# Performance work log

Measured on AMD Instinct MI355X. Metric: run time of the kernel, lower is better.

Reference implementation:

```python
import jax, jax.numpy as jnp
import numpy as np

H = 4
N = 1024
E = 4096
LE = 16384
FN = 128
FE = 64
FNO = 128
FEO = 64


def _lin(x, W, b):
    # torch nn.Linear: y = x @ W.T + b, W is [out, in]
    return x @ W.T + b


def setup_inputs() -> dict:
    key = jax.random.key(0)
    ks = jax.random.split(key, 24)
    s = 0.05
    inp = {}
    inp["node_inputs"] = jax.random.normal(ks[0], (N, FN), jnp.float32)
    inp["edge_inputs"] = jax.random.normal(ks[1], (E, FE), jnp.float32)
    inp["src"] = jax.random.randint(ks[2], (E,), 0, N, jnp.int32)
    inp["dst"] = jax.random.randint(ks[3], (E,), 0, N, jnp.int32)
    inp["lg_src"] = jax.random.randint(ks[4], (LE,), 0, E, jnp.int32)
    inp["lg_dst"] = jax.random.randint(ks[5], (LE,), 0, E, jnp.int32)
    # projection linear weights (torch Linear layout [out, in])
    inp["nqW"] = jax.random.normal(ks[6], (H * FN, FN), jnp.float32) * s
    inp["nqb"] = jax.random.normal(ks[7], (H * FN,), jnp.float32) * s
    inp["nkW"] = jax.random.normal(ks[8], (H, FN), jnp.float32) * s
    inp["nkb"] = jax.random.normal(ks[9], (H,), jnp.float32) * s
    inp["nvW"] = jax.random.normal(ks[10], (H * FN, FN), jnp.float32) * s
    inp["nvb"] = jax.random.normal(ks[11], (H * FN,), jnp.float32) * s
    inp["eqW"] = jax.random.normal(ks[12], (H * FE, FE), jnp.float32) * s
    inp["eqb"] = jax.random.normal(ks[13], (H * FE,), jnp.float32) * s
    inp["ekW"] = jax.random.normal(ks[14], (H, FE), jnp.float32) * s
    inp["ekb"] = jax.random.normal(ks[15], (H,), jnp.float32) * s
    inp["evW"] = jax.random.normal(ks[16], (H * FE, FE), jnp.float32) * s
    inp["evb"] = jax.random.normal(ks[17], (H * FE,), jnp.float32) * s
    # convolution output linears
    inp["ncW"] = jax.random.normal(ks[18], (FNO, FN), jnp.float32) * s
    inp["ncb"] = jax.random.normal(ks[19], (FNO,), jnp.float32) * s
    inp["ecW"] = jax.random.normal(ks[20], (FEO, FE), jnp.float32) * s
    inp["ecb"] = jax.random.normal(ks[21], (FEO,), jnp.float32) * s
    return inp


def reference(node_inputs, edge_inputs, src, dst, lg_src, lg_dst,
              nqW, nqb, nkW, nkb, nvW, nvb,
              eqW, eqb, ekW, ekb, evW, evb,
              ncW, ncb, ecW, ecb):
    n, fn = node_inputs.shape
    e, fe = edge_inputs.shape
    # per-head Q/K/V projections; .view(H, -1, F) == row-major reshape
    nq = _lin(node_inputs, nqW, nqb).reshape(H, -1, fn)   # [H,N,FN]
    nk = _lin(node_inputs, nkW, nkb).reshape(H, -1, 1)    # [H,N,1]
    nv = _lin(node_inputs, nvW, nvb).reshape(H, -1, fn)   # [H,N,FN]
    eq = _lin(edge_inputs, eqW, eqb).reshape(H, -1, fe)   # [H,E,FE]
    ek = _lin(edge_inputs, ekW, ekb).reshape(H, -1, 1)    # [H,E,1]
    ev = _lin(edge_inputs, evW, evb).reshape(H, -1, fe)   # [H,E,FE]
    # self attention: softmax(Q @ Q^T @ K, dim=1); associate as Q @ (Q^T K)
    node_sa = jax.nn.softmax(nq @ (jnp.swapaxes(nq, -1, -2) @ nk), axis=1)  # [H,N,1]
    edge_sa = jax.nn.softmax(eq @ (jnp.swapaxes(eq, -1, -2) @ ek), axis=1)  # [H,E,1]
    # vectorized edge-indexed scatter of attention scores into dense projections
    node_proj = jnp.zeros((H, n, n), node_inputs.dtype).at[:, src, dst].set(edge_sa[:, :, 0])
    conn = dst[lg_src]  # g.find_edges(source)[1]: destination node of edge lg_src
    edge_proj = jnp.zeros((H, e, e), edge_inputs.dtype).at[:, lg_src, lg_dst].set(node_sa[:, conn, 0])
    # dense adjacency matrices
    A = jnp.zeros((n, n), node_inputs.dtype).at[src, dst].set(1.0)
    Alg = jnp.zeros((e, e), edge_inputs.dtype).at[lg_src, lg_dst].set(1.0)
    # 'sum' aggregation: (attn_proj * A) @ value, then Linear + relu
    node_out = jax.nn.relu(_lin((node_proj * A) @ nv, ncW, ncb))   # [H,N,FNO]
    edge_out = jax.nn.relu(_lin((edge_proj * Alg) @ ev, ecW, ecb)) # [H,E,FEO]
    return (node_out, edge_out)
```

## Files before the change

kernel.cpp:

```cpp
#include <hip/hip_runtime.h>

#define H_ 4
#define N_ 1024
#define E_ 4096
#define LE_ 16384
#define FN_ 128
#define FE_ 64
#define CAP_ 32

struct P {
  const float *Xn, *Xe;
  const int *src, *dst, *lgs, *lgd;
  const float *nqW, *nqb, *nkW, *nkb, *nvW, *nvb;
  const float *eqW, *eqb, *ekW, *ekb, *evW, *evb;
  const float *ncW, *ncb, *ecW, *ecb;
  float *out;
  float *NV, *EV, *nsa, *esa;
  int *cntN, *cntE;
  int *listN, *listE;
  int *listNc, *listEc;
  int *degN, *degE;
};

template<int K, bool RELU>
__device__ void gemm_tile(const float* __restrict__ X, const float* __restrict__ W,
                          const float* __restrict__ b, float* __restrict__ C,
                          int O, int r0, int o0, float* smem, int t) {
  float* Xs = smem;
  float* Ws = smem + 2048;
  const int tn = t & 15, tm = t >> 4;
  float acc[4][4] = {};
  for (int k0 = 0; k0 < K; k0 += 32) {
#pragma unroll
    for (int ph = 0; ph < 2; ++ph) {
      int i4 = t + ph * 256;
      int m = i4 >> 3;
      int k4 = (i4 & 7) << 2;
      int m4 = m >> 2, ml = m & 3;
      float4 vx = *(const float4*)&X[(r0 + m) * K + k0 + k4];
      float4 vw = *(const float4*)&W[(o0 + m) * K + k0 + k4];
      Xs[(k4 + 0) * 64 + ((m4 ^ ((k4 + 0) & 15)) << 2) + ml] = vx.x;
      Xs[(k4 + 1) * 64 + ((m4 ^ ((k4 + 1) & 15)) << 2) + ml] = vx.y;
      Xs[(k4 + 2) * 64 + ((m4 ^ ((k4 + 2) & 15)) << 2) + ml] = vx.z;
      Xs[(k4 + 3) * 64 + ((m4 ^ ((k4 + 3) & 15)) << 2) + ml] = vx.w;
      Ws[(k4 + 0) * 64 + ((m4 ^ ((k4 + 0) & 15)) << 2) + ml] = vw.x;
      Ws[(k4 + 1) * 64 + ((m4 ^ ((k4 + 1) & 15)) << 2) + ml] = vw.y;
      Ws[(k4 + 2) * 64 + ((m4 ^ ((k4 + 2) & 15)) << 2) + ml] = vw.z;
      Ws[(k4 + 3) * 64 + ((m4 ^ ((k4 + 3) & 15)) << 2) + ml] = vw.w;
    }
    __syncthreads();
#pragma unroll
    for (int k = 0; k < 32; ++k) {
      float4 a = *(const float4*)&Xs[k * 64 + ((tm ^ (k & 15)) << 2)];
      float4 b4 = *(const float4*)&Ws[k * 64 + ((tn ^ (k & 15)) << 2)];
      acc[0][0] += a.x * b4.x; acc[0][1] += a.x * b4.y; acc[0][2] += a.x * b4.z; acc[0][3] += a.x * b4.w;
      acc[1][0] += a.y * b4.x; acc[1][1] += a.y * b4.y; acc[1][2] += a.y * b4.z; acc[1][3] += a.y * b4.w;
      acc[2][0] += a.z * b4.x; acc[2][1] += a.z * b4.y; acc[2][2] += a.z * b4.z; acc[2][3] += a.z * b4.w;
      acc[3][0] += a.w * b4.x; acc[3][1] += a.w * b4.y; acc[3][2] += a.w * b4.z; acc[3][3] += a.w * b4.w;
    }
    __syncthreads();
  }
  float4 bv = *(const float4*)&b[o0 + tn * 4];
#pragma unroll
  for (int i = 0; i < 4; ++i) {
    float4 o;
    o.x = acc[i][0] + bv.x; o.y = acc[i][1] + bv.y;
    o.z = acc[i][2] + bv.z; o.w = acc[i][3] + bv.w;
    if (RELU) {
      o.x = fmaxf(o.x, 0.f); o.y = fmaxf(o.y, 0.f);
      o.z = fmaxf(o.z, 0.f); o.w = fmaxf(o.w, 0.f);
    }
    *(float4*)&C[(r0 + tm * 4 + i) * O + o0 + tn * 4] = o;
  }
}

__global__ __launch_bounds__(1024) void A_attn(P p) {
  __shared__ float S[16384];
  const int tid = threadIdx.x, bid = blockIdx.x;

  if (bid >= 8) {
    int idx = (bid - 8) * 1024 + tid;
    if (idx < E_) {
      int e = idx, s = p.src[e], d = p.dst[e];
      int pos = atomicAdd(&p.cntN[s], 1);
      p.listN[s * CAP_ + ((unsigned)pos & (CAP_ - 1))] = (d << 12) | e;
    } else {
      int l = idx - E_, j = p.lgs[l], c = p.lgd[l];
      int pos = atomicAdd(&p.cntE[j], 1);
      p.listE[j * CAP_ + ((unsigned)pos & (CAP_ - 1))] = (c << 14) | l;
    }
    return;
  }

  float* ap0 = S;
  float* ap1 = S + 1024;
  float* ap2 = S + 2048;
  float* ap3 = S + 3072;
  float* sc   = S + 4096;
  float* knel = S + 8192;
  float* red  = S + 12288;
  float* ysp  = S + 13312;
  float* ts   = S + 13840;
  float* zs   = S + 13968;
  float* ds   = S + 14496;
  float* sig  = S + 14500;

  if (bid < 4) {
    const int h = bid;
    const int r0 = h * 256;
    {
      int rl = tid >> 2, c = tid & 3;
      const float4* x4 = (const float4*)(p.Xn + (r0 + rl) * FN_);
      const float4* w4 = (const float4*)(p.nkW + c * FN_);
      float acc = p.nkb[c];
      for (int k = 0; k < 32; ++k) {
        float4 x = x4[k], w = w4[k];
        acc += x.x * w.x + x.y * w.y + x.z * w.z + x.w * w.w;
      }
      knel[rl * 4 + c] = acc;
    }
    __syncthreads();
    {
      int g = tid & 127, q = tid >> 7;
      float a0 = 0, a1 = 0, a2 = 0, a3 = 0;
      for (int jj = 0; jj < 32; ++jj) {
        int rl = q * 32 + jj;
        float x = p.Xn[(r0 + rl) * FN_ + g];
        float4 k = ((float4*)knel)[rl];
        a0 += x * k.x; a1 += x * k.y; a2 += x * k.z; a3 += x * k.w;
      }
      ap0[tid] = a0; ap1[tid] = a1; ap2[tid] = a2; ap3[tid] = a3;
    }
    __syncthreads();
    for (int off = 512; off >= 128; off >>= 1) {
      if (tid < off) {
        ap0[tid] += ap0[tid + off]; ap1[tid] += ap1[tid + off];
        ap2[tid] += ap2[tid + off]; ap3[tid] += ap3[tid + off];
      }
      __syncthreads();
    }
    if (tid < 128) {
      ysp[0 * 132 + tid] = ap0[tid]; ysp[1 * 132 + tid] = ap1[tid];
      ysp[2 * 132 + tid] = ap2[tid]; ysp[3 * 132 + tid] = ap3[tid];
    }
    if (tid >= 128 && tid < 160) {
      int t2 = tid - 128, c = t2 & 3, part = t2 >> 2;
      float s = 0.f;
      for (int j = 0; j < 32; ++j) s += knel[(part * 32 + j) * 4 + c];
      red[t2] = s;
    }
    __syncthreads();
    if (tid < 4) { float s = 0.f; for (int q = 0; q < 8; ++q) s += red[q * 4 + tid]; sig[tid] = s; }
    __syncthreads();
    if (tid < 512) {
      const float4* w4 = (const float4*)(p.nqW + tid * FN_);
      int c = tid >> 7;
      const float* yc = ysp + c * 132;
      float s = 0.f;
      for (int g4 = 0; g4 < 32; ++g4) {
        float4 w = w4[g4];
        s += w.x * yc[g4 * 4 + 0] + w.y * yc[g4 * 4 + 1]
           + w.z * yc[g4 * 4 + 2] + w.w * yc[g4 * 4 + 3];
      }
      red[tid] = s;
    }
    __syncthreads();
    if (tid < 128) {
      float s = red[tid] + red[128 + tid] + red[256 + tid] + red[384 + tid];
      float bb = 0.f;
      for (int c = 0; c < 4; ++c) bb += p.nqb[c * 128 + tid] * sig[c];
      ts[tid] = s + bb;
    }
    __syncthreads();
    if (tid < 512) {
      int c = tid >> 7, g = tid & 127;
      float s = 0.f;
      for (int f = 0; f < 128; ++f) s += p.nqW[(c * 128 + f) * 128 + g] * ts[f];
      zs[c * 132 + g] = s;
    }
    if (tid >= 512 && tid < 516) {
      int c = tid - 512;
      float s = 0.f;
      for (int f = 0; f < 128; ++f) s += p.nqb[c * 128 + f] * ts[f];
      ds[c] = s;
    }
    __syncthreads();
    float scv;
    {
      int c = tid & 3, j = tid >> 2;
      const float4* x4 = (const float4*)(p.Xn + (r0 + j) * FN_);
      const float* z = zs + c * 132;
      float s = ds[c];
      for (int g4 = 0; g4 < 32; ++g4) {
        float4 x = x4[g4];
        s += x.x * z[g4 * 4] + x.y * z[g4 * 4 + 1] + x.z * z[g4 * 4 + 2] + x.w * z[g4 * 4 + 3];
      }
      scv = s;
    }
    red[tid] = scv;
    __syncthreads();
    for (int off = 512; off > 0; off >>= 1) {
      if (tid < off) red[tid] = fmaxf(red[tid], red[tid + off]);
      __syncthreads();
    }
    float m = red[0];
    __syncthreads();
    float e = expf(scv - m);
    red[tid] = e;
    __syncthreads();
    for (int off = 512; off > 0; off >>= 1) {
      if (tid < off) red[tid] += red[tid + off];
      __syncthreads();
    }
    p.nsa[h * N_ + tid] = e / red[0];
  } else {
    const int h = bid - 4;
    const int r0 = h * 1024;
    {
      const float4* x4 = (const float4*)(p.Xe + (r0 + tid) * FE_);
      const float4* w0 = (const float4*)(p.ekW);
      const float4* w1 = (const float4*)(p.ekW + 64);
      const float4* w2 = (const float4*)(p.ekW + 128);
      const float4* w3 = (const float4*)(p.ekW + 192);
      float a0 = p.ekb[0], a1 = p.ekb[1], a2 = p.ekb[2], a3 = p.ekb[3];
      for (int k = 0; k < 16; ++k) {
        float4 x = x4[k];
        float4 u0 = w0[k], u1 = w1[k], u2 = w2[k], u3 = w3[k];
        a0 += x.x * u0.x + x.y * u0.y + x.z * u0.z + x.w * u0.w;
        a1 += x.x * u1.x + x.y * u1.y + x.z * u1.z + x.w * u1.w;
        a2 += x.x * u2.x + x.y * u2.y + x.z * u2.z + x.w * u2.w;
        a3 += x.x * u3.x + x.y * u3.y + x.z * u3.z + x.w * u3.w;
      }
      ((float4*)knel)[tid] = make_float4(a0, a1, a2, a3);
    }
    __syncthreads();
    {
      int g = tid & 63, q = tid >> 6;
      float a0 = 0, a1 = 0, a2 = 0, a3 = 0;
      for (int jj = 0; jj < 64; ++jj) {
        int rl = q * 64 + jj;
        float x = p.Xe[(r0 + rl) * FE_ + g];
        float4 k = ((float4*)knel)[rl];
        a0 += x * k.x; a1 += x * k.y; a2 += x * k.z; a3 += x * k.w;
      }
      ap0[tid] = a0; ap1[tid] = a1; ap2[tid] = a2; ap3[tid] = a3;
    }
    __syncthreads();
    for (int off = 512; off >= 64; off >>= 1) {
      if (tid < off) {
        ap0[tid] += ap0[tid + off]; ap1[tid] += ap1[tid + off];
        ap2[tid] += ap2[tid + off]; ap3[tid] += ap3[tid + off];
      }
      __syncthreads();
    }
    if (tid < 64) {
      ysp[0 * 132 + tid] = ap0[tid]; ysp[1 * 132 + tid] = ap1[tid];
      ysp[2 * 132 + tid] = ap2[tid]; ysp[3 * 132 + tid] = ap3[tid];
    }
    if (tid >= 128 && tid < 160) {
      int t2 = tid - 128, c = t2 & 3, part = t2 >> 2;
      float s = 0.f;
      for (int j = 0; j < 128; ++j) s += knel[(r0 % 1 + part * 128 + j) * 4 + c];
      red[t2] = s;
    }
    __syncthreads();
    if (tid < 4) { float s = 0.f; for (int q = 0; q < 8; ++q) s += red[q * 4 + tid]; sig[tid] = s; }
    __syncthreads();
    if (tid < 256) {
      const float4* w4 = (const float4*)(p.eqW + tid * FE_);
      int c = tid >> 6;
      const float* yc = ysp + c * 132;
      float s = 0.f;
      for (int g4 = 0; g4 < 16; ++g4) {
        float4 w = w4[g4];
        s += w.x * yc[g4 * 4 + 0] + w.y * yc[g4 * 4 + 1]
           + w.z * yc[g4 * 4 + 2] + w.w * yc[g4 * 4 + 3];
      }
      red[tid] = s;
    }
    __syncthreads();
    if (tid < 64) {
      float s = red[tid] + red[64 + tid] + red[128 + tid] + red[192 + tid];
      float bb = 0.f;
      for (int c = 0; c < 4; ++c) bb += p.eqb[c * 64 + tid] * sig[c];
      ts[tid] = s + bb;
    }
    __syncthreads();
    if (tid < 256) {
      int c = tid >> 6, g = tid & 63;
      float s = 0.f;
      for (int f = 0; f < 64; ++f) s += p.eqW[(c * 64 + f) * 64 + g] * ts[f];
      zs[c * 132 + g] = s;
    }
    if (tid >= 256 && tid < 260) {
      int c = tid - 256;
      float s = 0.f;
      for (int f = 0; f < 64; ++f) s += p.eqb[c * 64 + f] * ts[f];
      ds[c] = s;
    }
    __syncthreads();
    float s4[4];
    {
      const float4* x4 = (const float4*)(p.Xe + (r0 + tid) * FE_);
      s4[0] = ds[0]; s4[1] = ds[1]; s4[2] = ds[2]; s4[3] = ds[3];
      for (int g4 = 0; g4 < 16; ++g4) {
        float4 x = x4[g4];
#pragma unroll
        for (int c = 0; c < 4; ++c) {
          const float* z = zs + c * 132 + g4 * 4;
          s4[c] += x.x * z[0] + x.y * z[1] + x.z * z[2] + x.w * z[3];
        }
      }
    }
    float lm = fmaxf(fmaxf(s4[0], s4[1]), fmaxf(s4[2], s4[3]));
    red[tid] = lm;
    __syncthreads();
    for (int off = 512; off > 0; off >>= 1) {
      if (tid < off) red[tid] = fmaxf(red[tid], red[tid + off]);
      __syncthreads();
    }
    float m = red[0];
    __syncthreads();
    float e0 = expf(s4[0] - m), e1 = expf(s4[1] - m);
    float e2 = expf(s4[2] - m), e3 = expf(s4[3] - m);
    red[tid] = e0 + e1 + e2 + e3;
    __syncthreads();
    for (int off = 512; off > 0; off >>= 1) {
      if (tid < off) red[tid] += red[tid + off];
      __syncthreads();
    }
    float inv = 1.f / red[0];
    ((float4*)(p.esa + h * E_))[tid] = make_float4(e0 * inv, e1 * inv, e2 * inv, e3 * inv);
  }
}

__global__ __launch_bounds__(256) void B_vproj(P p) {
  __shared__ float S[4096];
  const int t = threadIdx.x, bid = blockIdx.x;
  if (bid < 128) {
    gemm_tile<128, false>(p.Xn, p.nvW, p.nvb, p.NV, 512, (bid >> 3) * 64, (bid & 7) * 64, S, t);
  } else if (bid < 384) {
    int T2 = bid - 128;
    gemm_tile<64, false>(p.Xe, p.evW, p.evb, p.EV, 256, (T2 >> 2) * 64, (T2 & 3) * 64, S, t);
  } else {
    int idx = (bid - 384) * 256 + t;
    if (idx < N_) {
      int s = idx;
      unsigned base = (unsigned)p.cntN[N_];
      int deg = min((int)((unsigned)p.cntN[s] - base), CAP_);
      const int* lst = p.listN + s * CAP_;
      int* dstl = p.listNc + s * CAP_;
      int w = 0;
      for (int i = 0; i < deg; ++i) {
        int pk = lst[(base + i) & (CAP_ - 1)];
        bool win = true;
        for (int k2 = 0; k2 < deg; ++k2) {
          int pk2 = lst[(base + k2) & (CAP_ - 1)];
          if ((pk2 >> 12) == (pk >> 12) && pk2 > pk) win = false;
        }
        if (win) dstl[w++] = pk;
      }
      p.degN[s] = w;
    } else {
      int j = idx - N_;
      unsigned base = (unsigned)p.cntE[E_];
      int deg = min((int)((unsigned)p.cntE[j] - base), CAP_);
      const int* lst = p.listE + j * CAP_;
      int* dstl = p.listEc + j * CAP_;
      int w = 0;
      for (int i = 0; i < deg; ++i) {
        int pk = lst[(base + i) & (CAP_ - 1)];
        bool win = true;
        for (int k2 = 0; k2 < deg; ++k2) {
          int pk2 = lst[(base + k2) & (CAP_ - 1)];
          if ((pk2 >> 14) == (pk >> 14) && pk2 > pk) win = false;
        }
        if (win) dstl[w++] = pk;
      }
      p.degE[j] = w;
    }
  }
}

__global__ __launch_bounds__(256) void C_out(P p) {
  __shared__ float S[10240];
  const int t = threadIdx.x, bid = blockIdx.x;
  const int tn = t & 15, tm = t >> 4;
  float* Xs = S;

  if (bid < 128) {
    float* Ws = S + 8192;
    int rt = bid >> 1, o0 = (bid & 1) * 64;
    int r0 = rt * 64;
    int h = r0 >> 10, s0 = r0 & (N_ - 1);
    {
      int m = t >> 2, g0 = (t & 3) * 32;
      int m4 = m >> 2, ml = m & 3;
      int s = s0 + m;
      int deg = p.degN[s];
      const int* lst = p.listNc + s * CAP_;
      float acc[32];
#pragma unroll
      for (int c = 0; c < 32; ++c) acc[c] = 0.f;
      for (int i = 0; i < deg; ++i) {
        int pk = lst[i];
        int e = pk & (E_ - 1), d = pk >> 12;
        float a = p.esa[h * E_ + e];
        const float4* v4 = (const float4*)(p.NV + h * (N_ * FN_) + d * FN_ + g0);
#pragma unroll
        for (int c4 = 0; c4 < 8; ++c4) {
          float4 v = v4[c4];
          acc[c4 * 4 + 0] += a * v.x; acc[c4 * 4 + 1] += a * v.y;
          acc[c4 * 4 + 2] += a * v.z; acc[c4 * 4 + 3] += a * v.w;
        }
      }
#pragma unroll
      for (int c = 0; c < 32; ++c) {
        int k = g0 + c;
        Xs[k * 64 + ((m4 ^ (k & 15)) << 2) + ml] = acc[c];
      }
    }
    float accO[4][4] = {};
    for (int k0 = 0; k0 < 128; k0 += 32) {
      __syncthreads();
#pragma unroll
      for (int ph = 0; ph < 2; ++ph) {
        int i4 = t + ph * 256;
        int m = i4 >> 3, k4 = (i4 & 7) << 2;
        int m4 = m >> 2, ml = m & 3;
        float4 vw = *(const float4*)&p.ncW[(o0 + m) * 128 + k0 + k4];
        Ws[(k4 + 0) * 64 + ((m4 ^ ((k4 + 0) & 15)) << 2) + ml] = vw.x;
        Ws[(k4 + 1) * 64 + ((m4 ^ ((k4 + 1) & 15)) << 2) + ml] = vw.y;
        Ws[(k4 + 2) * 64 + ((m4 ^ ((k4 + 2) & 15)) << 2) + ml] = vw.z;
        Ws[(k4 + 3) * 64 + ((m4 ^ ((k4 + 3) & 15)) << 2) + ml] = vw.w;
      }
      __syncthreads();
#pragma unroll
      for (int k = 0; k < 32; ++k) {
        int ka = k0 + k;
        float4 a = *(const float4*)&Xs[ka * 64 + ((tm ^ (ka & 15)) << 2)];
        float4 b4 = *(const float4*)&Ws[k * 64 + ((tn ^ (k & 15)) << 2)];
        accO[0][0] += a.x * b4.x; accO[0][1] += a.x * b4.y; accO[0][2] += a.x * b4.z; accO[0][3] += a.x * b4.w;
        accO[1][0] += a.y * b4.x; accO[1][1] += a.y * b4.y; accO[1][2] += a.y * b4.z; accO[1][3] += a.y * b4.w;
        accO[2][0] += a.z * b4.x; accO[2][1] += a.z * b4.y; accO[2][2] += a.z * b4.z; accO[2][3] += a.z * b4.w;
        accO[3][0] += a.w * b4.x; accO[3][1] += a.w * b4.y; accO[3][2] += a.w * b4.z; accO[3][3] += a.w * b4.w;
      }
    }
    float4 bv = *(const float4*)&p.ncb[o0 + tn * 4];
#pragma unroll
    for (int i = 0; i < 4; ++i) {
      float4 o;
      o.x = fmaxf(accO[i][0] + bv.x, 0.f); o.y = fmaxf(accO[i][1] + bv.y, 0.f);
      o.z = fmaxf(accO[i][2] + bv.z, 0.f); o.w = fmaxf(accO[i][3] + bv.w, 0.f);
      *(float4*)&p.out[(r0 + tm * 4 + i) * 128 + o0 + tn * 4] = o;
    }
  } else {
    float* Ws = S + 4096;
    int T = bid - 128;
    int r0 = T * 64;
    int h = r0 >> 12, j0 = r0 & (E_ - 1);
    {
      int m = t >> 2, g0 = (t & 3) * 16;
      int m4 = m >> 2, ml = m & 3;
      int j = j0 + m;
      int deg = p.degE[j];
      const int* lst = p.listEc + j * CAP_;
      float acc[16];
#pragma unroll
      for (int c = 0; c < 16; ++c) acc[c] = 0.f;
      for (int i = 0; i < deg; ++i) {
        int c = lst[i] >> 14;
        const float4* v4 = (const float4*)(p.EV + h * (E_ * FE_) + c * FE_ + g0);
#pragma unroll
        for (int c4 = 0; c4 < 4; ++c4) {
          float4 v = v4[c4];
          acc[c4 * 4 + 0] += v.x; acc[c4 * 4 + 1] += v.y;
          acc[c4 * 4 + 2] += v.z; acc[c4 * 4 + 3] += v.w;
        }
      }
      float a = p.nsa[h * N_ + p.dst[j]];
#pragma unroll
      for (int c = 0; c < 16; ++c) {
        int k = g0 + c;
        Xs[k * 64 + ((m4 ^ (k & 15)) << 2) + ml] = a * acc[c];
      }
    }
    float accO[4][4] = {};
    for (int k0 = 0; k0 < 64; k0 += 32) {
      __syncthreads();
#pragma unroll
      for (int ph = 0; ph < 2; ++ph) {
        int i4 = t + ph * 256;
        int m = i4 >> 3, k4 = (i4 & 7) << 2;
        int m4 = m >> 2, ml = m & 3;
        float4 vw = *(const float4*)&p.ecW[m * 64 + k0 + k4];
        Ws[(k4 + 0) * 64 + ((m4 ^ ((k4 + 0) & 15)) << 2) + ml] = vw.x;
        Ws[(k4 + 1) * 64 + ((m4 ^ ((k4 + 1) & 15)) << 2) + ml] = vw.y;
        Ws[(k4 + 2) * 64 + ((m4 ^ ((k4 + 2) & 15)) << 2) + ml] = vw.z;
        Ws[(k4 + 3) * 64 + ((m4 ^ ((k4 + 3) & 15)) << 2) + ml] = vw.w;
      }
      __syncthreads();
#pragma unroll
      for (int k = 0; k < 32; ++k) {
        int ka = k0 + k;
        float4 a = *(const float4*)&Xs[ka * 64 + ((tm ^ (ka & 15)) << 2)];
        float4 b4 = *(const float4*)&Ws[k * 64 + ((tn ^ (k & 15)) << 2)];
        accO[0][0] += a.x * b4.x; accO[0][1] += a.x * b4.y; accO[0][2] += a.x * b4.z; accO[0][3] += a.x * b4.w;
        accO[1][0] += a.y * b4.x; accO[1][1] += a.y * b4.y; accO[1][2] += a.y * b4.z; accO[1][3] += a.y * b4.w;
        accO[2][0] += a.z * b4.x; accO[2][1] += a.z * b4.y; accO[2][2] += a.z * b4.z; accO[2][3] += a.z * b4.w;
        accO[3][0] += a.w * b4.x; accO[3][1] += a.w * b4.y; accO[3][2] += a.w * b4.z; accO[3][3] += a.w * b4.w;
      }
    }
    float4 bv = *(const float4*)&p.ecb[tn * 4];
    float* outE = p.out + (size_t)H_ * N_ * 128;
#pragma unroll
    for (int i = 0; i < 4; ++i) {
      float4 o;
      o.x = fmaxf(accO[i][0] + bv.x, 0.f); o.y = fmaxf(accO[i][1] + bv.y, 0.f);
      o.z = fmaxf(accO[i][2] + bv.z, 0.f); o.w = fmaxf(accO[i][3] + bv.w, 0.f);
      *(float4*)&outE[(r0 + tm * 4 + i) * 64 + tn * 4] = o;
    }
  }
}

extern "C" void kernel_launch(void* const* d_in, const int* in_sizes, int n_in,
                              void* d_out, int out_size, void* d_ws, size_t ws_size,
                              hipStream_t stream) {
  P p;
  p.Xn  = (const float*)d_in[0];
  p.Xe  = (const float*)d_in[1];
  p.src = (const int*)d_in[2];
  p.dst = (const int*)d_in[3];
  p.lgs = (const int*)d_in[4];
  p.lgd = (const int*)d_in[5];
  p.nqW = (const float*)d_in[6];  p.nqb = (const float*)d_in[7];
  p.nkW = (const float*)d_in[8];  p.nkb = (const float*)d_in[9];
  p.nvW = (const float*)d_in[10]; p.nvb = (const float*)d_in[11];
  p.eqW = (const float*)d_in[12]; p.eqb = (const float*)d_in[13];
  p.ekW = (const float*)d_in[14]; p.ekb = (const float*)d_in[15];
  p.evW = (const float*)d_in[16]; p.evb = (const float*)d_in[17];
  p.ncW = (const float*)d_in[18]; p.ncb = (const float*)d_in[19];
  p.ecW = (const float*)d_in[20]; p.ecb = (const float*)d_in[21];
  p.out = (float*)d_out;

  float* f = (float*)d_ws;
  p.NV    = f; f += N_ * H_ * FN_;
  p.EV    = f; f += E_ * H_ * FE_;
  p.nsa   = f; f += H_ * N_;
  p.esa   = f; f += H_ * E_;
  p.cntN  = (int*)f; f += N_ + 1;
  p.cntE  = (int*)f; f += E_ + 1;
  p.listN = (int*)f; f += N_ * CAP_;
  p.listE = (int*)f; f += E_ * CAP_;
  p.listNc = (int*)f; f += N_ * CAP_;
  p.listEc = (int*)f; f += E_ * CAP_;
  p.degN  = (int*)f; f += N_;
  p.degE  = (int*)f; f += E_;

  A_attn<<<28, 1024, 0, stream>>>(p);
  B_vproj<<<404, 256, 0, stream>>>(p);
  C_out<<<384, 256, 0, stream>>>(p);
}
```

Before: 183.6 us.

## Split attention reduction across many blocks and co-schedule with value projections

```diff
diff --git a/kernel.cpp b/kernel.cpp
--- a/kernel.cpp
+++ b/kernel.cpp
@@ -16,6 +16,7 @@
   const float *ncW, *ncb, *ecW, *ecb;
   float *out;
   float *NV, *EV, *nsa, *esa;
+  float *ypN, *ypE, *sgN, *sgE;
   int *cntN, *cntE;
   int *listN, *listE;
   int *listNc, *listEc;
@@ -74,12 +75,115 @@
   }
 }
 
-__global__ __launch_bounds__(1024) void A_attn(P p) {
-  __shared__ float S[16384];
-  const int tid = threadIdx.x, bid = blockIdx.x;
-
-  if (bid >= 8) {
-    int idx = (bid - 8) * 1024 + tid;
+__global__ __launch_bounds__(256) void K1(P p) {
+  __shared__ float S[4096];
+  const int t = threadIdx.x, bid = blockIdx.x;
+
+  if (bid < 128) {
+    gemm_tile<128, false>(p.Xn, p.nvW, p.nvb, p.NV, 512, (bid >> 3) * 64, (bid & 7) * 64, S, t);
+    return;
+  }
+  if (bid < 384) {
+    int T2 = bid - 128;
+    gemm_tile<64, false>(p.Xe, p.evW, p.evb, p.EV, 256, (T2 >> 2) * 64, (T2 & 3) * 64, S, t);
+    return;
+  }
+  if (bid < 416) {
+    int z = bid - 384;
+    int h = z >> 3, ch = z & 7;
+    int r0c = h * 256 + ch * 32;
+    float* knel = S;
+    float* ap0 = S + 128;
+    float* ap1 = S + 384;
+    float* ap2 = S + 640;
+    float* ap3 = S + 896;
+    if (t < 128) {
+      int rl = t >> 2, c = t & 3;
+      const float4* x4 = (const float4*)(p.Xn + (r0c + rl) * FN_);
+      const float4* w4 = (const float4*)(p.nkW + c * FN_);
+      float acc = p.nkb[c];
+      for (int k = 0; k < 32; ++k) {
+        float4 x = x4[k], w = w4[k];
+        acc += x.x * w.x + x.y * w.y + x.z * w.z + x.w * w.w;
+      }
+      knel[t] = acc;
+    }
+    __syncthreads();
+    {
+      int g = t & 127, q = t >> 7;
+      float a0 = 0, a1 = 0, a2 = 0, a3 = 0;
+      for (int jj = 0; jj < 16; ++jj) {
+        int rl = q * 16 + jj;
+        float x = p.Xn[(r0c + rl) * FN_ + g];
+        float4 k = ((float4*)knel)[rl];
+        a0 += x * k.x; a1 += x * k.y; a2 += x * k.z; a3 += x * k.w;
+      }
+      ap0[t] = a0; ap1[t] = a1; ap2[t] = a2; ap3[t] = a3;
+    }
+    __syncthreads();
+    if (t < 128) {
+      float* yp = p.ypN + z * 528;
+      yp[0 * 132 + t] = ap0[t] + ap0[128 + t];
+      yp[1 * 132 + t] = ap1[t] + ap1[128 + t];
+      yp[2 * 132 + t] = ap2[t] + ap2[128 + t];
+      yp[3 * 132 + t] = ap3[t] + ap3[128 + t];
+    } else if (t < 132) {
+      int c = t - 128;
+      float s = 0.f;
+      for (int rl = 0; rl < 32; ++rl) s += knel[rl * 4 + c];
+      p.sgN[z * 4 + c] = s;
+    }
+    return;
+  }
+  if (bid < 480) {
+    int z = bid - 416;
+    int h = z >> 4, ch = z & 15;
+    int r0c = h * 1024 + ch * 64;
+    float* knel = S;
+    float* ap0 = S + 256;
+    float* ap1 = S + 512;
+    float* ap2 = S + 768;
+    float* ap3 = S + 1024;
+    {
+      int rl = t >> 2, c = t & 3;
+      const float4* x4 = (const float4*)(p.Xe + (r0c + rl) * FE_);
+      const float4* w4 = (const float4*)(p.ekW + c * FE_);
+      float acc = p.ekb[c];
+      for (int k = 0; k < 16; ++k) {
+        float4 x = x4[k], w = w4[k];
+        acc += x.x * w.x + x.y * w.y + x.z * w.z + x.w * w.w;
+      }
+      knel[t] = acc;
+    }
+    __syncthreads();
+    {
+      int g = t & 63, q = t >> 6;
+      float a0 = 0, a1 = 0, a2 = 0, a3 = 0;
+      for (int jj = 0; jj < 16; ++jj) {
+        int rl = q * 16 + jj;
+        float x = p.Xe[(r0c + rl) * FE_ + g];
+        float4 k = ((float4*)knel)[rl];
+        a0 += x * k.x; a1 += x * k.y; a2 += x * k.z; a3 += x * k.w;
+      }
+      ap0[t] = a0; ap1[t] = a1; ap2[t] = a2; ap3[t] = a3;
+    }
+    __syncthreads();
+    if (t < 64) {
+      float* yp = p.ypE + z * 528;
+      yp[0 * 132 + t] = ap0[t] + ap0[64 + t] + ap0[128 + t] + ap0[192 + t];
+      yp[1 * 132 + t] = ap1[t] + ap1[64 + t] + ap1[128 + t] + ap1[192 + t];
+      yp[2 * 132 + t] = ap2[t] + ap2[64 + t] + ap2[128 + t] + ap2[192 + t];
+      yp[3 * 132 + t] = ap3[t] + ap3[64 + t] + ap3[128 + t] + ap3[192 + t];
+    } else if (t < 68) {
+      int c = t - 64;
+      float s = 0.f;
+      for (int rl = 0; rl < 64; ++rl) s += knel[rl * 4 + c];
+      p.sgE[z * 4 + c] = s;
+    }
+    return;
+  }
+  {
+    int idx = (bid - 480) * 256 + t;
     if (idx < E_) {
       int e = idx, s = p.src[e], d = p.dst[e];
       int pos = atomicAdd(&p.cntN[s], 1);
@@ -89,261 +193,20 @@
       int pos = atomicAdd(&p.cntE[j], 1);
       p.listE[j * CAP_ + ((unsigned)pos & (CAP_ - 1))] = (c << 14) | l;
     }
-    return;
-  }
-
-  float* ap0 = S;
-  float* ap1 = S + 1024;
-  float* ap2 = S + 2048;
-  float* ap3 = S + 3072;
-  float* sc   = S + 4096;
-  float* knel = S + 8192;
-  float* red  = S + 12288;
-  float* ysp  = S + 13312;
-  float* ts   = S + 13840;
-  float* zs   = S + 13968;
-  float* ds   = S + 14496;
-  float* sig  = S + 14500;
-
-  if (bid < 4) {
-    const int h = bid;
-    const int r0 = h * 256;
-    {
-      int rl = tid >> 2, c = tid & 3;
-      const float4* x4 = (const float4*)(p.Xn + (r0 + rl) * FN_);
-      const float4* w4 = (const float4*)(p.nkW + c * FN_);
-      float acc = p.nkb[c];
-      for (int k = 0; k < 32; ++k) {
-        float4 x = x4[k], w = w4[k];
-        acc += x.x * w.x + x.y * w.y + x.z * w.z + x.w * w.w;
-      }
-      knel[rl * 4 + c] = acc;
-    }
-    __syncthreads();
-    {
-      int g = tid & 127, q = tid >> 7;
-      float a0 = 0, a1 = 0, a2 = 0, a3 = 0;
-      for (int jj = 0; jj < 32; ++jj) {
-        int rl = q * 32 + jj;
-        float x = p.Xn[(r0 + rl) * FN_ + g];
-        float4 k = ((float4*)knel)[rl];
-        a0 += x * k.x; a1 += x * k.y; a2 += x * k.z; a3 += x * k.w;
-      }
-      ap0[tid] = a0; ap1[tid] = a1; ap2[tid] = a2; ap3[tid] = a3;
-    }
-    __syncthreads();
-    for (int off = 512; off >= 128; off >>= 1) {
-      if (tid < off) {
-        ap0[tid] += ap0[tid + off]; ap1[tid] += ap1[tid + off];
-        ap2[tid] += ap2[tid + off]; ap3[tid] += ap3[tid + off];
-      }
-      __syncthreads();
-    }
-    if (tid < 128) {
-      ysp[0 * 132 + tid] = ap0[tid]; ysp[1 * 132 + tid] = ap1[tid];
-      ysp[2 * 132 + tid] = ap2[tid]; ysp[3 * 132 + tid] = ap3[tid];
-    }
-    if (tid >= 128 && tid < 160) {
-      int t2 = tid - 128, c = t2 & 3, part = t2 >> 2;
-      float s = 0.f;
-      for (int j = 0; j < 32; ++j) s += knel[(part * 32 + j) * 4 + c];
-      red[t2] = s;
-    }
-    __syncthreads();
-    if (tid < 4) { float s = 0.f; for (int q = 0; q < 8; ++q) s += red[q * 4 + tid]; sig[tid] = s; }
-    __syncthreads();
-    if (tid < 512) {
-      const float4* w4 = (const float4*)(p.nqW + tid * FN_);
-      int c = tid >> 7;
-      const float* yc = ysp + c * 132;
-      float s = 0.f;
-      for (int g4 = 0; g4 < 32; ++g4) {
-        float4 w = w4[g4];
-        s += w.x * yc[g4 * 4 + 0] + w.y * yc[g4 * 4 + 1]
-           + w.z * yc[g4 * 4 + 2] + w.w * yc[g4 * 4 + 3];
-      }
-      red[tid] = s;
-    }
-    __syncthreads();
-    if (tid < 128) {
-      float s = red[tid] + red[128 + tid] + red[256 + tid] + red[384 + tid];
-      float bb = 0.f;
-      for (int c = 0; c < 4; ++c) bb += p.nqb[c * 128 + tid] * sig[c];
-      ts[tid] = s + bb;
-    }
-    __syncthreads();
-    if (tid < 512) {
-      int c = tid >> 7, g = tid & 127;
-      float s = 0.f;
-      for (int f = 0; f < 128; ++f) s += p.nqW[(c * 128 + f) * 128 + g] * ts[f];
-      zs[c * 132 + g] = s;
-    }
-    if (tid >= 512 && tid < 516) {
-      int c = tid - 512;
-      float s = 0.f;
-      for (int f = 0; f < 128; ++f) s += p.nqb[c * 128 + f] * ts[f];
-      ds[c] = s;
-    }
-    __syncthreads();
-    float scv;
-    {
-      int c = tid & 3, j = tid >> 2;
-      const float4* x4 = (const float4*)(p.Xn + (r0 + j) * FN_);
-      const float* z = zs + c * 132;
-      float s = ds[c];
-      for (int g4 = 0; g4 < 32; ++g4) {
-        float4 x = x4[g4];
-        s += x.x * z[g4 * 4] + x.y * z[g4 * 4 + 1] + x.z * z[g4 * 4 + 2] + x.w * z[g4 * 4 + 3];
-      }
-      scv = s;
-    }
-    red[tid] = scv;
-    __syncthreads();
-    for (int off = 512; off > 0; off >>= 1) {
-      if (tid < off) red[tid] = fmaxf(red[tid], red[tid + off]);
-      __syncthreads();
-    }
-    float m = red[0];
-    __syncthreads();
-    float e = expf(scv - m);
-    red[tid] = e;
-    __syncthreads();
-    for (int off = 512; off > 0; off >>= 1) {
-      if (tid < off) red[tid] += red[tid + off];
-      __syncthreads();
-    }
-    p.nsa[h * N_ + tid] = e / red[0];
-  } else {
-    const int h = bid - 4;
-    const int r0 = h * 1024;
-    {
-      const float4* x4 = (const float4*)(p.Xe + (r0 + tid) * FE_);
-      const float4* w0 = (const float4*)(p.ekW);
-      const float4* w1 = (const float4*)(p.ekW + 64);
-      const float4* w2 = (const float4*)(p.ekW + 128);
-      const float4* w3 = (const float4*)(p.ekW + 192);
-      float a0 = p.ekb[0], a1 = p.ekb[1], a2 = p.ekb[2], a3 = p.ekb[3];
-      for (int k = 0; k < 16; ++k) {
-        float4 x = x4[k];
-        float4 u0 = w0[k], u1 = w1[k], u2 = w2[k], u3 = w3[k];
-        a0 += x.x * u0.x + x.y * u0.y + x.z * u0.z + x.w * u0.w;
-        a1 += x.x * u1.x + x.y * u1.y + x.z * u1.z + x.w * u1.w;
-        a2 += x.x * u2.x + x.y * u2.y + x.z * u2.z + x.w * u2.w;
-        a3 += x.x * u3.x + x.y * u3.y + x.z * u3.z + x.w * u3.w;
-      }
-      ((float4*)knel)[tid] = make_float4(a0, a1, a2, a3);
-    }
-    __syncthreads();
-    {
-      int g = tid & 63, q = tid >> 6;
-      float a0 = 0, a1 = 0, a2 = 0, a3 = 0;
-      for (int jj = 0; jj < 64; ++jj) {
-        int rl = q * 64 + jj;
-        float x = p.Xe[(r0 + rl) * FE_ + g];
-        float4 k = ((float4*)knel)[rl];
-        a0 += x * k.x; a1 += x * k.y; a2 += x * k.z; a3 += x * k.w;
-      }
-      ap0[tid] = a0; ap1[tid] = a1; ap2[tid] = a2; ap3[tid] = a3;
-    }
-    __syncthreads();
-    for (int off = 512; off >= 64; off >>= 1) {
-      if (tid < off) {
-        ap0[tid] += ap0[tid + off]; ap1[tid] += ap1[tid + off];
-        ap2[tid] += ap2[tid + off]; ap3[tid] += ap3[tid + off];
-      }
-      __syncthreads();
-    }
-    if (tid < 64) {
-      ysp[0 * 132 + tid] = ap0[tid]; ysp[1 * 132 + tid] = ap1[tid];
-      ysp[2 * 132 + tid] = ap2[tid]; ysp[3 * 132 + tid] = ap3[tid];
-    }
-    if (tid >= 128 && tid < 160) {
-      int t2 = tid - 128, c = t2 & 3, part = t2 >> 2;
-      float s = 0.f;
-      for (int j = 0; j < 128; ++j) s += knel[(r0 % 1 + part * 128 + j) * 4 + c];
-      red[t2] = s;
-    }
-    __syncthreads();
-    if (tid < 4) { float s = 0.f; for (int q = 0; q < 8; ++q) s += red[q * 4 + tid]; sig[tid] = s; }
-    __syncthreads();
-    if (tid < 256) {
-      const float4* w4 = (const float4*)(p.eqW + tid * FE_);
-      int c = tid >> 6;
-      const float* yc = ysp + c * 132;
-      float s = 0.f;
-      for (int g4 = 0; g4 < 16; ++g4) {
-        float4 w = w4[g4];
-        s += w.x * yc[g4 * 4 + 0] + w.y * yc[g4 * 4 + 1]
-           + w.z * yc[g4 * 4 + 2] + w.w * yc[g4 * 4 + 3];
-      }
-      red[tid] = s;
-    }
-    __syncthreads();
-    if (tid < 64) {
-      float s = red[tid] + red[64 + tid] + red[128 + tid] + red[192 + tid];
-      float bb = 0.f;
-      for (int c = 0; c < 4; ++c) bb += p.eqb[c * 64 + tid] * sig[c];
-      ts[tid] = s + bb;
-    }
-    __syncthreads();
-    if (tid < 256) {
-      int c = tid >> 6, g = tid & 63;
-      float s = 0.f;
-      for (int f = 0; f < 64; ++f) s += p.eqW[(c * 64 + f) * 64 + g] * ts[f];
-      zs[c * 132 + g] = s;
-    }
-    if (tid >= 256 && tid < 260) {
-      int c = tid - 256;
-      float s = 0.f;
-      for (int f = 0; f < 64; ++f) s += p.eqb[c * 64 + f] * ts[f];
-      ds[c] = s;
-    }
-    __syncthreads();
-    float s4[4];
-    {
-      const float4* x4 = (const float4*)(p.Xe + (r0 + tid) * FE_);
-      s4[0] = ds[0]; s4[1] = ds[1]; s4[2] = ds[2]; s4[3] = ds[3];
-      for (int g4 = 0; g4 < 16; ++g4) {
-        float4 x = x4[g4];
-#pragma unroll
-        for (int c = 0; c < 4; ++c) {
-          const float* z = zs + c * 132 + g4 * 4;
-          s4[c] += x.x * z[0] + x.y * z[1] + x.z * z[2] + x.w * z[3];
-        }
-      }
-    }
-    float lm = fmaxf(fmaxf(s4[0], s4[1]), fmaxf(s4[2], s4[3]));
-    red[tid] = lm;
-    __syncthreads();
-    for (int off = 512; off > 0; off >>= 1) {
-      if (tid < off) red[tid] = fmaxf(red[tid], red[tid + off]);
-      __syncthreads();
-    }
-    float m = red[0];
-    __syncthreads();
-    float e0 = expf(s4[0] - m), e1 = expf(s4[1] - m);
-    float e2 = expf(s4[2] - m), e3 = expf(s4[3] - m);
-    red[tid] = e0 + e1 + e2 + e3;
-    __syncthreads();
-    for (int off = 512; off > 0; off >>= 1) {
-      if (tid < off) red[tid] += red[tid + off];
-      __syncthreads();
-    }
-    float inv = 1.f / red[0];
-    ((float4*)(p.esa + h * E_))[tid] = make_float4(e0 * inv, e1 * inv, e2 * inv, e3 * inv);
   }
 }
 
-__global__ __launch_bounds__(256) void B_vproj(P p) {
-  __shared__ float S[4096];
-  const int t = threadIdx.x, bid = blockIdx.x;
-  if (bid < 128) {
-    gemm_tile<128, false>(p.Xn, p.nvW, p.nvb, p.NV, 512, (bid >> 3) * 64, (bid & 7) * 64, S, t);
-  } else if (bid < 384) {
-    int T2 = bid - 128;
-    gemm_tile<64, false>(p.Xe, p.evW, p.evb, p.EV, 256, (T2 >> 2) * 64, (T2 & 3) * 64, S, t);
-  } else {
-    int idx = (bid - 384) * 256 + t;
+__global__ __launch_bounds__(1024) void K2(P p) {
+  __shared__ float red[1024];
+  __shared__ float ysp[528];
+  __shared__ float ts[128];
+  __shared__ float zs[528];
+  __shared__ float ds[4], sig[4];
+  const int tid = threadIdx.x, bid = blockIdx.x;
+
+  if (bid >= 8) {
+    int idx = (bid - 8) * 1024 + tid;
+    if (idx >= N_ + E_) return;
     if (idx < N_) {
       int s = idx;
       unsigned base = (unsigned)p.cntN[N_];
@@ -379,19 +242,177 @@
       }
       p.degE[j] = w;
     }
+    return;
+  }
+
+  if (bid < 4) {
+    const int h = bid;
+    const int r0 = h * 256;
+    if (tid < 512) {
+      int c = tid >> 7, g = tid & 127;
+      float s = 0.f;
+      for (int ch = 0; ch < 8; ++ch) s += p.ypN[(h * 8 + ch) * 528 + c * 132 + g];
+      ysp[c * 132 + g] = s;
+    } else if (tid < 516) {
+      int c = tid - 512;
+      float s = 0.f;
+      for (int ch = 0; ch < 8; ++ch) s += p.sgN[(h * 8 + ch) * 4 + c];
+      sig[c] = s;
+    }
+    __syncthreads();
+    if (tid < 512) {
+      const float4* w4 = (const float4*)(p.nqW + tid * FN_);
+      int c = tid >> 7;
+      const float* yc = ysp + c * 132;
+      float s = 0.f;
+      for (int g4 = 0; g4 < 32; ++g4) {
+        float4 w = w4[g4];
+        s += w.x * yc[g4 * 4 + 0] + w.y * yc[g4 * 4 + 1]
+           + w.z * yc[g4 * 4 + 2] + w.w * yc[g4 * 4 + 3];
+      }
+      red[tid] = s;
+    }
+    __syncthreads();
+    if (tid < 128) {
+      float s = red[tid] + red[128 + tid] + red[256 + tid] + red[384 + tid];
+      float bb = 0.f;
+      for (int c = 0; c < 4; ++c) bb += p.nqb[c * 128 + tid] * sig[c];
+      ts[tid] = s + bb;
+    }
+    __syncthreads();
+    if (tid < 512) {
+      int c = tid >> 7, g = tid & 127;
+      float s = 0.f;
+      for (int f = 0; f < 128; ++f) s += p.nqW[(c * 128 + f) * 128 + g] * ts[f];
+      zs[c * 132 + g] = s;
+    }
+    if (tid >= 512 && tid < 516) {
+      int c = tid - 512;
+      float s = 0.f;
+      for (int f = 0; f < 128; ++f) s += p.nqb[c * 128 + f] * ts[f];
+      ds[c] = s;
+    }
+    __syncthreads();
+    float scv;
+    {
+      int c = tid & 3, j = tid >> 2;
+      const float4* x4 = (const float4*)(p.Xn + (r0 + j) * FN_);
+      const float* z = zs + c * 132;
+      float s = ds[c];
+      for (int g4 = 0; g4 < 32; ++g4) {
+        float4 x = x4[g4];
+        s += x.x * z[g4 * 4] + x.y * z[g4 * 4 + 1] + x.z * z[g4 * 4 + 2] + x.w * z[g4 * 4 + 3];
+      }
+      scv = s;
+    }
+    red[tid] = scv;
+    __syncthreads();
+    for (int off = 512; off > 0; off >>= 1) {
+      if (tid < off) red[tid] = fmaxf(red[tid], red[tid + off]);
+      __syncthreads();
+    }
+    float m = red[0];
+    __syncthreads();
+    float e = expf(scv - m);
+    red[tid] = e;
+    __syncthreads();
+    for (int off = 512; off > 0; off >>= 1) {
+      if (tid < off) red[tid] += red[tid + off];
+      __syncthreads();
+    }
+    p.nsa[h * N_ + tid] = e / red[0];
+  } else {
+    const int h = bid - 4;
+    const int r0 = h * 1024;
+    if (tid < 256) {
+      int c = tid >> 6, g = tid & 63;
+      float s = 0.f;
+      for (int ch = 0; ch < 16; ++ch) s += p.ypE[(h * 16 + ch) * 528 + c * 132 + g];
+      ysp[c * 132 + g] = s;
+    } else if (tid < 260) {
+      int c = tid - 256;
+      float s = 0.f;
+      for (int ch = 0; ch < 16; ++ch) s += p.sgE[(h * 16 + ch) * 4 + c];
+      sig[c] = s;
+    }
+    __syncthreads();
+    if (tid < 256) {
+      const float4* w4 = (const float4*)(p.eqW + tid * FE_);
+      int c = tid >> 6;
+      const float* yc = ysp + c * 132;
+      float s = 0.f;
+      for (int g4 = 0; g4 < 16; ++g4) {
+        float4 w = w4[g4];
+        s += w.x * yc[g4 * 4 + 0] + w.y * yc[g4 * 4 + 1]
+           + w.z * yc[g4 * 4 + 2] + w.w * yc[g4 * 4 + 3];
+      }
+      red[tid] = s;
+    }
+    __syncthreads();
+    if (tid < 64) {
+      float s = red[tid] + red[64 + tid] + red[128 + tid] + red[192 + tid];
+      float bb = 0.f;
+      for (int c = 0; c < 4; ++c) bb += p.eqb[c * 64 + tid] * sig[c];
+      ts[tid] = s + bb;
+    }
+    __syncthreads();
+    if (tid < 256) {
+      int c = tid >> 6, g = tid & 63;
+      float s = 0.f;
+      for (int f = 0; f < 64; ++f) s += p.eqW[(c * 64 + f) * 64 + g] * ts[f];
+      zs[c * 132 + g] = s;
+    }
+    if (tid >= 256 && tid < 260) {
+      int c = tid - 256;
+      float s = 0.f;
+      for (int f = 0; f < 64; ++f) s += p.eqb[c * 64 + f] * ts[f];
+      ds[c] = s;
+    }
+    __syncthreads();
+    float s4[4];
+    {
+      const float4* x4 = (const float4*)(p.Xe + (r0 + tid) * FE_);
+      s4[0] = ds[0]; s4[1] = ds[1]; s4[2] = ds[2]; s4[3] = ds[3];
+      for (int g4 = 0; g4 < 16; ++g4) {
+        float4 x = x4[g4];
+#pragma unroll
+        for (int c = 0; c < 4; ++c) {
+          const float* z = zs + c * 132 + g4 * 4;
+          s4[c] += x.x * z[0] + x.y * z[1] + x.z * z[2] + x.w * z[3];
+        }
+      }
+    }
+    float lm = fmaxf(fmaxf(s4[0], s4[1]), fmaxf(s4[2], s4[3]));
+    red[tid] = lm;
+    __syncthreads();
+    for (int off = 512; off > 0; off >>= 1) {
+      if (tid < off) red[tid] = fmaxf(red[tid], red[tid + off]);
+      __syncthreads();
+    }
+    float m = red[0];
+    __syncthreads();
+    float e0 = expf(s4[0] - m), e1 = expf(s4[1] - m);
+    float e2 = expf(s4[2] - m), e3 = expf(s4[3] - m);
+    red[tid] = e0 + e1 + e2 + e3;
+    __syncthreads();
+    for (int off = 512; off > 0; off >>= 1) {
+      if (tid < off) red[tid] += red[tid + off];
+      __syncthreads();
+    }
+    float inv = 1.f / red[0];
+    ((float4*)(p.esa + h * E_))[tid] = make_float4(e0 * inv, e1 * inv, e2 * inv, e3 * inv);
   }
 }
 
-__global__ __launch_bounds__(256) void C_out(P p) {
+__global__ __launch_bounds__(256) void K3(P p) {
   __shared__ float S[10240];
   const int t = threadIdx.x, bid = blockIdx.x;
   const int tn = t & 15, tm = t >> 4;
   float* Xs = S;
 
-  if (bid < 128) {
+  if (bid < 64) {
     float* Ws = S + 8192;
-    int rt = bid >> 1, o0 = (bid & 1) * 64;
-    int r0 = rt * 64;
+    int r0 = bid * 64;
     int h = r0 >> 10, s0 = r0 & (N_ - 1);
     {
       int m = t >> 2, g0 = (t & 3) * 32;
@@ -420,43 +441,50 @@
         Xs[k * 64 + ((m4 ^ (k & 15)) << 2) + ml] = acc[c];
       }
     }
-    float accO[4][4] = {};
-    for (int k0 = 0; k0 < 128; k0 += 32) {
-      __syncthreads();
-#pragma unroll
-      for (int ph = 0; ph < 2; ++ph) {
-        int i4 = t + ph * 256;
-        int m = i4 >> 3, k4 = (i4 & 7) << 2;
-        int m4 = m >> 2, ml = m & 3;
-        float4 vw = *(const float4*)&p.ncW[(o0 + m) * 128 + k0 + k4];
-        Ws[(k4 + 0) * 64 + ((m4 ^ ((k4 + 0) & 15)) << 2) + ml] = vw.x;
-        Ws[(k4 + 1) * 64 + ((m4 ^ ((k4 + 1) & 15)) << 2) + ml] = vw.y;
-        Ws[(k4 + 2) * 64 + ((m4 ^ ((k4 + 2) & 15)) << 2) + ml] = vw.z;
-        Ws[(k4 + 3) * 64 + ((m4 ^ ((k4 + 3) & 15)) << 2) + ml] = vw.w;
-      }
-      __syncthreads();
-#pragma unroll
-      for (int k = 0; k < 32; ++k) {
-        int ka = k0 + k;
-        float4 a = *(const float4*)&Xs[ka * 64 + ((tm ^ (ka & 15)) << 2)];
-        float4 b4 = *(const float4*)&Ws[k * 64 + ((tn ^ (k & 15)) << 2)];
-        accO[0][0] += a.x * b4.x; accO[0][1] += a.x * b4.y; accO[0][2] += a.x * b4.z; accO[0][3] += a.x * b4.w;
-        accO[1][0] += a.y * b4.x; accO[1][1] += a.y * b4.y; accO[1][2] += a.y * b4.z; accO[1][3] += a.y * b4.w;
-        accO[2][0] += a.z * b4.x; accO[2][1] += a.z * b4.y; accO[2][2] += a.z * b4.z; accO[2][3] += a.z * b4.w;
-        accO[3][0] += a.w * b4.x; accO[3][1] += a.w * b4.y; accO[3][2] += a.w * b4.z; accO[3][3] += a.w * b4.w;
-      }
-    }
-    float4 bv = *(const float4*)&p.ncb[o0 + tn * 4];
-#pragma unroll
-    for (int i = 0; i < 4; ++i) {
-      float4 o;
-      o.x = fmaxf(accO[i][0] + bv.x, 0.f); o.y = fmaxf(accO[i][1] + bv.y, 0.f);
-      o.z = fmaxf(accO[i][2] + bv.z, 0.f); o.w = fmaxf(accO[i][3] + bv.w, 0.f);
-      *(float4*)&p.out[(r0 + tm * 4 + i) * 128 + o0 + tn * 4] = o;
+    float accO[4][8] = {};
+#pragma unroll
+    for (int oh = 0; oh < 2; ++oh) {
+      int o0 = oh * 64;
+      for (int k0 = 0; k0 < 128; k0 += 32) {
+        __syncthreads();
+#pragma unroll
+        for (int ph = 0; ph < 2; ++ph) {
+          int i4 = t + ph * 256;
+          int m = i4 >> 3, k4 = (i4 & 7) << 2;
+          int m4 = m >> 2, ml = m & 3;
+          float4 vw = *(const float4*)&p.ncW[(o0 + m) * 128 + k0 + k4];
+          Ws[(k4 + 0) * 64 + ((m4 ^ ((k4 + 0) & 15)) << 2) + ml] = vw.x;
+          Ws[(k4 + 1) * 64 + ((m4 ^ ((k4 + 1) & 15)) << 2) + ml] = vw.y;
+          Ws[(k4 + 2) * 64 + ((m4 ^ ((k4 + 2) & 15)) << 2) + ml] = vw.z;
+          Ws[(k4 + 3) * 64 + ((m4 ^ ((k4 + 3) & 15)) << 2) + ml] = vw.w;
+        }
+        __syncthreads();
+#pragma unroll
+        for (int k = 0; k < 32; ++k) {
+          int ka = k0 + k;
+          float4 a = *(const float4*)&Xs[ka * 64 + ((tm ^ (ka & 15)) << 2)];
+          float4 b4 = *(const float4*)&Ws[k * 64 + ((tn ^ (k & 15)) << 2)];
+          accO[0][oh*4+0] += a.x * b4.x; accO[0][oh*4+1] += a.x * b4.y; accO[0][oh*4+2] += a.x * b4.z; accO[0][oh*4+3] += a.x * b4.w;
+          accO[1][oh*4+0] += a.y * b4.x; accO[1][oh*4+1] += a.y * b4.y; accO[1][oh*4+2] += a.y * b4.z; accO[1][oh*4+3] += a.y * b4.w;
+          accO[2][oh*4+0] += a.z * b4.x; accO[2][oh*4+1] += a.z * b4.y; accO[2][oh*4+2] += a.z * b4.z; accO[2][oh*4+3] += a.z * b4.w;
+          accO[3][oh*4+0] += a.w * b4.x; accO[3][oh*4+1] += a.w * b4.y; accO[3][oh*4+2] += a.w * b4.z; accO[3][oh*4+3] += a.w * b4.w;
+        }
+      }
+    }
+#pragma unroll
+    for (int oh = 0; oh < 2; ++oh) {
+      float4 bv = *(const float4*)&p.ncb[oh * 64 + tn * 4];
+#pragma unroll
+      for (int i = 0; i < 4; ++i) {
+        float4 o;
+        o.x = fmaxf(accO[i][oh*4+0] + bv.x, 0.f); o.y = fmaxf(accO[i][oh*4+1] + bv.y, 0.f);
+        o.z = fmaxf(accO[i][oh*4+2] + bv.z, 0.f); o.w = fmaxf(accO[i][oh*4+3] + bv.w, 0.f);
+        *(float4*)&p.out[(r0 + tm * 4 + i) * 128 + oh * 64 + tn * 4] = o;
+      }
     }
   } else {
     float* Ws = S + 4096;
-    int T = bid - 128;
+    int T = bid - 64;
     int r0 = T * 64;
     int h = r0 >> 12, j0 = r0 & (E_ - 1);
     {
@@ -548,6 +576,10 @@
   p.EV    = f; f += E_ * H_ * FE_;
   p.nsa   = f; f += H_ * N_;
   p.esa   = f; f += H_ * E_;
+  p.ypN   = f; f += 32 * 528;
+  p.ypE   = f; f += 64 * 528;
+  p.sgN   = f; f += 32 * 4;
+  p.sgE   = f; f += 64 * 4;
   p.cntN  = (int*)f; f += N_ + 1;
   p.cntE  = (int*)f; f += E_ + 1;
   p.listN = (int*)f; f += N_ * CAP_;
@@ -557,7 +589,7 @@
   p.degN  = (int*)f; f += N_;
   p.degE  = (int*)f; f += E_;
 
-  A_attn<<<28, 1024, 0, stream>>>(p);
-  B_vproj<<<404, 256, 0, stream>>>(p);
-  C_out<<<384, 256, 0, stream>>>(p);
+  K1<<<560, 256, 0, stream>>>(p);
+  K2<<<13, 1024, 0, stream>>>(p);
+  K3<<<320, 256, 0, stream>>>(p);
 }
```

After: 166.4 us. 1.1x faster.
